# Kernel tuning notes

Hardware: AMD Instinct MI355X
Metric: run time of the kernel (lower is better)

Reference implementation:

```python
import jax, jax.numpy as jnp
import numpy as np

IMG_SIZE = 640
STRIDES = (8, 16, 32)
KA = 3          # anchors per level
C = 80          # num classes
CONF_THRESH = 0.001
NMS_THRESH = 0.6
TOPK = 4096     # fixed candidate cap for jit-compatible NMS


def setup_inputs() -> dict:
    key = jax.random.key(0)
    k1, k2, k3 = jax.random.split(key, 3)
    ch = KA * (1 + C + 4)  # 255
    pred_s = jax.random.normal(k1, (ch, 80, 80), dtype=jnp.float32)
    pred_m = jax.random.normal(k2, (ch, 40, 40), dtype=jnp.float32)
    pred_l = jax.random.normal(k3, (ch, 20, 20), dtype=jnp.float32)
    # classic YOLOv3 anchors, [level, anchor, (w,h)]
    anchor_size = jnp.array(
        [[[10, 13], [16, 30], [33, 23]],
         [[30, 61], [62, 45], [59, 119]],
         [[116, 90], [156, 198], [373, 326]]], dtype=jnp.float32)
    return {"pred_s": pred_s, "pred_m": pred_m, "pred_l": pred_l,
            "anchor_size": anchor_size}


def _decode_level(pred, anchors, stride):
    # pred: [KA*(1+C+4), H, W]; anchors: [KA, 2]
    H, W = pred.shape[1], pred.shape[2]
    p = jnp.transpose(pred, (1, 2, 0))                    # [H, W, ch]
    obj = p[..., :KA].reshape(-1, 1)                      # [H*W*KA, 1]
    cls = p[..., KA:KA * (1 + C)].reshape(-1, C)          # [H*W*KA, C]
    reg = p[..., KA * (1 + C):].reshape(H * W, KA, 4)     # [H*W, KA, 4]
    gy, gx = jnp.meshgrid(jnp.arange(H), jnp.arange(W), indexing="ij")
    grid = jnp.stack([gx, gy], -1).reshape(-1, 1, 2).astype(pred.dtype)  # [H*W,1,2]
    # center_sample = False branch
    xy = (jax.nn.sigmoid(reg[..., :2]) + grid) * stride
    wh = jnp.exp(reg[..., 2:]) * anchors[None, :, :]
    box = jnp.concatenate([xy - 0.5 * wh, xy + 0.5 * wh], -1).reshape(-1, 4)
    return obj, cls, box


def _decode(pred_s, pred_m, pred_l, anchor_size):
    parts = [_decode_level(p, anchor_size[i], STRIDES[i])
             for i, p in enumerate([pred_s, pred_m, pred_l])]
    obj = jnp.concatenate([p[0] for p in parts], 0)       # [N,1]
    cls = jnp.concatenate([p[1] for p in parts], 0)       # [N,C]
    box = jnp.concatenate([p[2] for p in parts], 0)       # [N,4]
    bboxes = jnp.clip(box / IMG_SIZE, 0.0, 1.0)
    scores = jax.nn.sigmoid(obj) * jax.nn.softmax(cls, axis=-1)
    return bboxes, scores


def reference(pred_s, pred_m, pred_l, anchor_size):
    bboxes, scores = _decode(pred_s, pred_m, pred_l, anchor_size)
    cls_inds = jnp.argmax(scores, axis=1)                 # [N]
    sc = jnp.max(scores, axis=1)                          # [N]
    sc_masked = jnp.where(sc >= CONF_THRESH, sc, -1.0)
    top_sc, idx = jax.lax.top_k(sc_masked, TOPK)          # candidates, score-sorted
    b = bboxes[idx]                                       # [K,4]
    c = cls_inds[idx]                                     # [K]
    valid = top_sc >= CONF_THRESH                         # [K]
    # pairwise IoU, exactly as the numpy NMS computes it
    x1, y1, x2, y2 = b[:, 0], b[:, 1], b[:, 2], b[:, 3]
    area = (x2 - x1) * (y2 - y1)
    xx1 = jnp.maximum(x1[:, None], x1[None, :])
    yy1 = jnp.maximum(y1[:, None], y1[None, :])
    xx2 = jnp.minimum(x2[:, None], x2[None, :])
    yy2 = jnp.minimum(y2[:, None], y2[None, :])
    w = jnp.maximum(1e-28, xx2 - xx1)
    h = jnp.maximum(1e-28, yy2 - yy1)
    inter = w * h
    iou = inter / (area[:, None] + area[None, :] - inter + 1e-14)
    # sup[j, i] = kept j (earlier in score order) suppresses i, same class only
    order = jnp.arange(TOPK)
    sup = (c[:, None] == c[None, :]) & (iou > NMS_THRESH) \
          & (order[:, None] < order[None, :])
    def body(i, keep):
        ki = valid[i] & ~jnp.any(keep & sup[:, i])
        return keep.at[i].set(ki)
    keep = jax.lax.fori_loop(0, TOPK, body, jnp.zeros(TOPK, dtype=bool))
    return b, top_sc, c, keep
```

## Files before the change

### kernel.cpp

```cpp
#include <hip/hip_runtime.h>
#include <cstdint>
#include <cstddef>

#define N_ANCH 25200
#define NB0 19200
#define NB1 24000
#define TOPK_N 4096
#define CONF_T 0.001
#define NMS_T 0.6
#define IMGS 640.0
#define NBINS 8192
#define JS 16

typedef unsigned long long u64;

struct WS {
  alignas(64) double sc[N_ANCH];
  alignas(64) double box[N_ANCH][4];
  alignas(64) int    cls[N_ANCH];
  alignas(64) int    binv[N_ANCH];
  alignas(64) int    rank[N_ANCH];
  alignas(64) int    subset[N_ANCH];
  alignas(64) double ssc[N_ANCH];
  int    m_count;
  int    t_bin;
  alignas(64) double tbox[TOPK_N][4];
  alignas(64) double tarea[TOPK_N];
  alignas(64) double tsc[TOPK_N];
  alignas(64) int    tcls[TOPK_N];
  alignas(64) u64    supT[TOPK_N * 64];
  alignas(64) u64    hasSup[64];
};

__device__ __forceinline__ double dsigmoid(double x) { return 1.0 / (1.0 + exp(-x)); }

__device__ __forceinline__ int score_bin(double sc) {
  if (sc < 0.0) return 0;
  return (int)(__float_as_uint((float)sc) >> 17);
}

__global__ void k_decode(const float* __restrict__ ps, const float* __restrict__ pm,
                         const float* __restrict__ pl, const float* __restrict__ anch,
                         WS* __restrict__ ws) {
  int tid = blockIdx.x * 256 + threadIdx.x;
  int a = tid >> 2;
  int r = tid & 3;
  if (a >= N_ANCH) return;
  const float* p; int W, base, lvl; double stride;
  if (a < NB0)      { p = ps; W = 80; base = 0;   lvl = 0; stride = 8.0; }
  else if (a < NB1) { p = pm; W = 40; base = NB0; lvl = 1; stride = 16.0; }
  else              { p = pl; W = 20; base = NB1; lvl = 2; stride = 32.0; }
  int e = a - base;
  int pos = e / 3;
  int k = e - 3 * pos;
  int HW = W * W;

  const float* pc = p + (size_t)(3 + k * 80) * HW + pos;
  double m = -1e300, ssum = 0.0; int am = 0;
  for (int t = 0; t < 20; ++t) {
    int c = r + 4 * t;
    double v = (double)pc[(size_t)c * HW];
    ssum += exp(v);
    if (v > m) { m = v; am = c; }
  }
  for (int off = 1; off <= 2; off <<= 1) {
    double om = __shfl_xor(m, off);
    int oam   = __shfl_xor(am, off);
    double os = __shfl_xor(ssum, off);
    ssum += os;
    if (om > m || (om == m && oam < am)) { m = om; am = oam; }
  }

  if (r == 0) {
    double sobj = dsigmoid((double)p[(size_t)k * HW + pos]);
    double sc = sobj * (exp(m) / ssum);

    int x = pos % W, y = pos / W;
    const float* pr = p + (size_t)(243 + k * 4) * HW + pos;
    double tx = (double)pr[0];
    double ty = (double)pr[(size_t)HW];
    double tw = (double)pr[(size_t)2 * HW];
    double th = (double)pr[(size_t)3 * HW];
    double cx = (dsigmoid(tx) + (double)x) * stride;
    double cy = (dsigmoid(ty) + (double)y) * stride;
    double aw = (double)anch[lvl * 6 + k * 2 + 0];
    double ah = (double)anch[lvl * 6 + k * 2 + 1];
    double bw = exp(tw) * aw;
    double bh = exp(th) * ah;
    double x1 = fmin(fmax((cx - 0.5 * bw) / IMGS, 0.0), 1.0);
    double y1 = fmin(fmax((cy - 0.5 * bh) / IMGS, 0.0), 1.0);
    double x2 = fmin(fmax((cx + 0.5 * bw) / IMGS, 0.0), 1.0);
    double y2 = fmin(fmax((cy + 0.5 * bh) / IMGS, 0.0), 1.0);

    ws->box[a][0] = x1; ws->box[a][1] = y1;
    ws->box[a][2] = x2; ws->box[a][3] = y2;
    ws->cls[a] = am;
    double scm = (sc >= CONF_T) ? sc : -1.0;
    ws->sc[a] = scm;
    ws->binv[a] = score_bin(scm);
  }
}

__global__ void __launch_bounds__(1024) k_select(WS* __restrict__ ws) {
  __shared__ int hist[NBINS];
  __shared__ int part[1024];
  int t = threadIdx.x;
  for (int i = t; i < NBINS; i += 1024) hist[i] = 0;
  __syncthreads();
  for (int i = t; i < N_ANCH; i += 1024) atomicAdd(&hist[ws->binv[i]], 1);
  __syncthreads();
  const int CH = NBINS / 1024;
  int sum = 0;
  for (int rr = 0; rr < CH; ++rr) sum += hist[NBINS - 1 - (t * CH + rr)];
  part[t] = sum;
  __syncthreads();
  for (int off = 1; off < 1024; off <<= 1) {
    int v = (t >= off) ? part[t - off] : 0;
    __syncthreads();
    part[t] += v;
    __syncthreads();
  }
  int cum = part[t] - sum;
  for (int rr = 0; rr < CH; ++rr) {
    int b = NBINS - 1 - (t * CH + rr);
    int h = hist[b];
    int prev = cum;
    cum += h;
    if (prev < TOPK_N && cum >= TOPK_N) ws->t_bin = b;
  }
  if (t == 0) ws->m_count = 0;
}

__global__ void k_compact(WS* __restrict__ ws) {
  int i = blockIdx.x * 256 + threadIdx.x;
  if (i < 64) ws->hasSup[i] = 0ull;
  if (i >= N_ANCH) return;
  int tb = ws->t_bin;
  if (ws->binv[i] >= tb) {
    int idx = atomicAdd(&ws->m_count, 1);
    ws->subset[idx] = i;
    ws->ssc[idx] = ws->sc[i];
    ws->rank[idx] = 0;
  }
}

__global__ void k_rank(WS* __restrict__ ws) {
  const int CHUNK = 1024;
  __shared__ double sj[CHUNK];
  __shared__ int    aj[CHUNK];
  int m = ws->m_count;
  if ((int)blockIdx.x * 256 >= m) return;
  int i = blockIdx.x * 256 + threadIdx.x;
  bool active = (i < m);
  int ai = active ? ws->subset[i] : 0;
  double si = active ? ws->ssc[i] : -2.0;

  int jlen = (m + JS - 1) / JS;
  int j0 = blockIdx.y * jlen;
  int jend = min(j0 + jlen, m);
  int cnt = 0;
  for (int jc = j0; jc < jend; jc += CHUNK) {
    int n = min(CHUNK, jend - jc);
    __syncthreads();
    for (int t = threadIdx.x; t < n; t += 256) {
      aj[t] = ws->subset[jc + t];
      sj[t] = ws->ssc[jc + t];
    }
    __syncthreads();
    if (active) {
      for (int t = 0; t < n; ++t) {
        double s = sj[t];
        cnt += (int)((s > si) | ((s == si) & (aj[t] < ai)));
      }
    }
  }
  if (active && cnt) atomicAdd(&ws->rank[i], cnt);
}

__global__ void k_scatter(WS* __restrict__ ws, float* __restrict__ out) {
  int m = ws->m_count;
  int i = blockIdx.x * 256 + threadIdx.x;
  if (i >= m) return;
  int r = ws->rank[i];
  if (r >= TOPK_N) return;
  int a = ws->subset[i];
  double b0 = ws->box[a][0], b1 = ws->box[a][1];
  double b2 = ws->box[a][2], b3 = ws->box[a][3];
  double s  = ws->ssc[i];
  int    c  = ws->cls[a];
  ws->tbox[r][0] = b0; ws->tbox[r][1] = b1;
  ws->tbox[r][2] = b2; ws->tbox[r][3] = b3;
  ws->tarea[r] = (b2 - b0) * (b3 - b1);
  ws->tsc[r] = s;
  ws->tcls[r] = c;
  out[r * 4 + 0] = (float)b0;
  out[r * 4 + 1] = (float)b1;
  out[r * 4 + 2] = (float)b2;
  out[r * 4 + 3] = (float)b3;
  out[4 * TOPK_N + r] = (float)s;
  out[5 * TOPK_N + r] = (float)c;
}

__global__ void k_iou(WS* __restrict__ ws) {
  int tid = threadIdx.x;
  int w = blockIdx.y;
  int i0 = blockIdx.x * 256;
  int jbase = w * 64;
  if (jbase >= i0 + 256) {
    ws->supT[(size_t)(i0 + tid) * 64 + w] = 0ull;
    return;
  }
  __shared__ double jb[64][5];
  __shared__ int jc[64];
  if (tid < 64) {
    int j = jbase + tid;
    jb[tid][0] = ws->tbox[j][0];
    jb[tid][1] = ws->tbox[j][1];
    jb[tid][2] = ws->tbox[j][2];
    jb[tid][3] = ws->tbox[j][3];
    jb[tid][4] = ws->tarea[j];
    jc[tid] = ws->tcls[j];
  }
  __syncthreads();
  int i = i0 + tid;
  double x1 = ws->tbox[i][0], y1 = ws->tbox[i][1];
  double x2 = ws->tbox[i][2], y2 = ws->tbox[i][3];
  double ai = ws->tarea[i];
  int ci = ws->tcls[i];
  u64 bits = 0;
  for (int t = 0; t < 64; ++t) {
    double xx1 = fmax(x1, jb[t][0]);
    double yy1 = fmax(y1, jb[t][1]);
    double xx2 = fmin(x2, jb[t][2]);
    double yy2 = fmin(y2, jb[t][3]);
    double iw = fmax(1e-28, xx2 - xx1);
    double ih = fmax(1e-28, yy2 - yy1);
    double inter = iw * ih;
    double denom = ai + jb[t][4] - inter + 1e-14;
    bool sup = (jc[t] == ci) && (inter > NMS_T * denom) && ((jbase + t) < i);
    bits |= ((u64)sup) << t;
  }
  ws->supT[(size_t)i * 64 + w] = bits;
  if (bits) atomicOr(&ws->hasSup[i >> 6], 1ull << (i & 63));
}

__global__ void __launch_bounds__(64) k_nms(const WS* __restrict__ ws, float* __restrict__ out) {
  __shared__ u64 hsArr[64];
  __shared__ int lst[TOPK_N];
  int lane = threadIdx.x;

  u64 validw = 0;
  const double4* tp = (const double4*)(ws->tsc + lane * 64);
  for (int q = 0; q < 16; ++q) {
    double4 v = tp[q];
    validw |= ((u64)(v.x >= CONF_T)) << (q * 4 + 0);
    validw |= ((u64)(v.y >= CONF_T)) << (q * 4 + 1);
    validw |= ((u64)(v.z >= CONF_T)) << (q * 4 + 2);
    validw |= ((u64)(v.w >= CONF_T)) << (q * 4 + 3);
  }

  u64 hasw = ws->hasSup[lane];
  u64 keepw = validw & ~hasw;
  hsArr[lane] = hasw;
  __syncthreads();

  int K = 0;
  for (int l = 0; l < 64; ++l) {
    u64 w = hsArr[l];
    while (w) {
      int b = __builtin_ctzll(w);
      w &= w - 1;
      if (lane == 0) lst[K] = l * 64 + b;
      ++K;
    }
  }
  __syncthreads();

  const u64* ST = ws->supT;
  int IA[16], IB[16];
  u64 A[16], B[16];

#pragma unroll
  for (int r = 0; r < 16; ++r) IA[r] = (r < K) ? lst[r] : 0;
#pragma unroll
  for (int r = 0; r < 16; ++r) A[r] = (r < K) ? ST[(size_t)IA[r] * 64 + lane] : 0ull;

  for (int base = 0; base < K; base += 32) {
#pragma unroll
    for (int r = 0; r < 16; ++r) IB[r] = (base + 16 + r < K) ? lst[base + 16 + r] : 0;
#pragma unroll
    for (int r = 0; r < 16; ++r) B[r] = (base + 16 + r < K) ? ST[(size_t)IB[r] * 64 + lane] : 0ull;
#pragma unroll
    for (int r = 0; r < 16; ++r) {
      if (base + r < K) {
        int i = IA[r];
        u64 bal = __ballot((keepw & A[r]) != 0ull);
        if (lane == (i >> 6) && bal == 0ull && ((validw >> (i & 63)) & 1ull))
          keepw |= 1ull << (i & 63);
      }
    }
#pragma unroll
    for (int r = 0; r < 16; ++r) IA[r] = (base + 32 + r < K) ? lst[base + 32 + r] : 0;
#pragma unroll
    for (int r = 0; r < 16; ++r) A[r] = (base + 32 + r < K) ? ST[(size_t)IA[r] * 64 + lane] : 0ull;
#pragma unroll
    for (int r = 0; r < 16; ++r) {
      if (base + 16 + r < K) {
        int i = IB[r];
        u64 bal = __ballot((keepw & B[r]) != 0ull);
        if (lane == (i >> 6) && bal == 0ull && ((validw >> (i & 63)) & 1ull))
          keepw |= 1ull << (i & 63);
      }
    }
  }

  for (int b = 0; b < 64; ++b)
    out[6 * TOPK_N + lane * 64 + b] = (float)((keepw >> b) & 1ull);
}

extern "C" void kernel_launch(void* const* d_in, const int* in_sizes, int n_in,
                              void* d_out, int out_size, void* d_ws, size_t ws_size,
                              hipStream_t stream) {
  const float* ps   = (const float*)d_in[0];
  const float* pm   = (const float*)d_in[1];
  const float* pl   = (const float*)d_in[2];
  const float* anch = (const float*)d_in[3];
  float* out = (float*)d_out;
  WS* ws = (WS*)d_ws;

  dim3 blk(256);
  k_decode <<<dim3((N_ANCH * 4 + 255) / 256), blk, 0, stream>>>(ps, pm, pl, anch, ws);
  k_select <<<dim3(1), dim3(1024), 0, stream>>>(ws);
  k_compact<<<dim3((N_ANCH + 255) / 256), blk, 0, stream>>>(ws);
  k_rank   <<<dim3((N_ANCH + 255) / 256, JS), blk, 0, stream>>>(ws);
  k_scatter<<<dim3((N_ANCH + 255) / 256), blk, 0, stream>>>(ws, out);
  k_iou    <<<dim3(TOPK_N / 256, 64), blk, 0, stream>>>(ws);
  k_nms    <<<dim3(1), dim3(64), 0, stream>>>(ws, out);
}
```

Before: 123.6 us.

## Fuse all seven stages into one cooperative persistent kernel with grid syncs

Replaces the seven separate launches (decode, select, compact, rank, scatter, iou, nms) with a single cooperative kernel of 256 blocks that separates phases with grid.sync(). The histogram becomes a two-level one, with per-block shared histograms merged into a global one, and every block redoes the prefix scan to find the threshold bin locally. The rank stage is remapped so each thread handles up to three candidates. This targets the launch overhead and the gaps between the many small dependent kernels, at the cost of grid-wide barriers and lower parallelism in the decode and rank phases.

```diff
diff --git a/kernel.cpp b/kernel.cpp
--- a/kernel.cpp
+++ b/kernel.cpp
@@ -1,6 +1,9 @@
 #include <hip/hip_runtime.h>
+#include <hip/hip_cooperative_groups.h>
 #include <cstdint>
 #include <cstddef>
+
+namespace cg = cooperative_groups;
 
 #define N_ANCH 25200
 #define NB0 19200
@@ -10,7 +13,8 @@
 #define NMS_T 0.6
 #define IMGS 640.0
 #define NBINS 8192
-#define JS 16
+#define GRID_B 256
+#define NTHR (GRID_B * 256)
 
 typedef unsigned long long u64;
 
@@ -22,8 +26,8 @@
   alignas(64) int    rank[N_ANCH];
   alignas(64) int    subset[N_ANCH];
   alignas(64) double ssc[N_ANCH];
+  alignas(64) int    hist[NBINS];
   int    m_count;
-  int    t_bin;
   alignas(64) double tbox[TOPK_N][4];
   alignas(64) double tarea[TOPK_N];
   alignas(64) double tsc[TOPK_N];
@@ -39,283 +43,307 @@
   return (int)(__float_as_uint((float)sc) >> 17);
 }
 
-__global__ void k_decode(const float* __restrict__ ps, const float* __restrict__ pm,
-                         const float* __restrict__ pl, const float* __restrict__ anch,
-                         WS* __restrict__ ws) {
-  int tid = blockIdx.x * 256 + threadIdx.x;
-  int a = tid >> 2;
-  int r = tid & 3;
-  if (a >= N_ANCH) return;
-  const float* p; int W, base, lvl; double stride;
-  if (a < NB0)      { p = ps; W = 80; base = 0;   lvl = 0; stride = 8.0; }
-  else if (a < NB1) { p = pm; W = 40; base = NB0; lvl = 1; stride = 16.0; }
-  else              { p = pl; W = 20; base = NB1; lvl = 2; stride = 32.0; }
-  int e = a - base;
-  int pos = e / 3;
-  int k = e - 3 * pos;
-  int HW = W * W;
-
-  const float* pc = p + (size_t)(3 + k * 80) * HW + pos;
-  double m = -1e300, ssum = 0.0; int am = 0;
-  for (int t = 0; t < 20; ++t) {
-    int c = r + 4 * t;
-    double v = (double)pc[(size_t)c * HW];
-    ssum += exp(v);
-    if (v > m) { m = v; am = c; }
-  }
-  for (int off = 1; off <= 2; off <<= 1) {
-    double om = __shfl_xor(m, off);
-    int oam   = __shfl_xor(am, off);
-    double os = __shfl_xor(ssum, off);
-    ssum += os;
-    if (om > m || (om == m && oam < am)) { m = om; am = oam; }
-  }
-
-  if (r == 0) {
-    double sobj = dsigmoid((double)p[(size_t)k * HW + pos]);
-    double sc = sobj * (exp(m) / ssum);
-
-    int x = pos % W, y = pos / W;
-    const float* pr = p + (size_t)(243 + k * 4) * HW + pos;
-    double tx = (double)pr[0];
-    double ty = (double)pr[(size_t)HW];
-    double tw = (double)pr[(size_t)2 * HW];
-    double th = (double)pr[(size_t)3 * HW];
-    double cx = (dsigmoid(tx) + (double)x) * stride;
-    double cy = (dsigmoid(ty) + (double)y) * stride;
-    double aw = (double)anch[lvl * 6 + k * 2 + 0];
-    double ah = (double)anch[lvl * 6 + k * 2 + 1];
-    double bw = exp(tw) * aw;
-    double bh = exp(th) * ah;
-    double x1 = fmin(fmax((cx - 0.5 * bw) / IMGS, 0.0), 1.0);
-    double y1 = fmin(fmax((cy - 0.5 * bh) / IMGS, 0.0), 1.0);
-    double x2 = fmin(fmax((cx + 0.5 * bw) / IMGS, 0.0), 1.0);
-    double y2 = fmin(fmax((cy + 0.5 * bh) / IMGS, 0.0), 1.0);
-
-    ws->box[a][0] = x1; ws->box[a][1] = y1;
-    ws->box[a][2] = x2; ws->box[a][3] = y2;
-    ws->cls[a] = am;
-    double scm = (sc >= CONF_T) ? sc : -1.0;
-    ws->sc[a] = scm;
-    ws->binv[a] = score_bin(scm);
-  }
-}
-
-__global__ void __launch_bounds__(1024) k_select(WS* __restrict__ ws) {
-  __shared__ int hist[NBINS];
-  __shared__ int part[1024];
-  int t = threadIdx.x;
-  for (int i = t; i < NBINS; i += 1024) hist[i] = 0;
+struct SelSmem { int hist[NBINS]; int part[256]; };
+struct RankSmem { double sj[2048]; int aj[2048]; };
+struct IouSmem { double jb[64][5]; int jc[64]; };
+struct NmsSmem { u64 hs[64]; int lst[TOPK_N]; };
+
+__global__ void __launch_bounds__(256)
+k_fused(const float* __restrict__ ps, const float* __restrict__ pm,
+        const float* __restrict__ pl, const float* __restrict__ anch,
+        WS* __restrict__ ws, float* __restrict__ out) {
+  cg::grid_group grid = cg::this_grid();
+  __shared__ union { SelSmem sel; RankSmem rk; IouSmem iou; NmsSmem nms; } sm;
+  __shared__ int s_tbin;
+
+  const int t = threadIdx.x;
+  const int gtid = blockIdx.x * 256 + t;
+
+  for (int b = gtid; b < NBINS; b += NTHR) ws->hist[b] = 0;
+  if (gtid < 64) ws->hasSup[gtid] = 0ull;
+  if (gtid == 64) ws->m_count = 0;
+
+  for (int task = gtid; task < N_ANCH * 4; task += NTHR) {
+    int a = task >> 2;
+    int r = task & 3;
+    const float* p; int W, base, lvl; double stride;
+    if (a < NB0)      { p = ps; W = 80; base = 0;   lvl = 0; stride = 8.0; }
+    else if (a < NB1) { p = pm; W = 40; base = NB0; lvl = 1; stride = 16.0; }
+    else              { p = pl; W = 20; base = NB1; lvl = 2; stride = 32.0; }
+    int e = a - base;
+    int pos = e / 3;
+    int k = e - 3 * pos;
+    int HW = W * W;
+
+    const float* pc = p + (size_t)(3 + k * 80) * HW + pos;
+    double m = -1e300, ssum = 0.0; int am = 0;
+    for (int u = 0; u < 20; ++u) {
+      int c = r + 4 * u;
+      double v = (double)pc[(size_t)c * HW];
+      ssum += exp(v);
+      if (v > m) { m = v; am = c; }
+    }
+    for (int off = 1; off <= 2; off <<= 1) {
+      double om = __shfl_xor(m, off);
+      int oam   = __shfl_xor(am, off);
+      double os = __shfl_xor(ssum, off);
+      ssum += os;
+      if (om > m || (om == m && oam < am)) { m = om; am = oam; }
+    }
+
+    if (r == 0) {
+      double sobj = dsigmoid((double)p[(size_t)k * HW + pos]);
+      double sc = sobj * (exp(m) / ssum);
+
+      int x = pos % W, y = pos / W;
+      const float* pr = p + (size_t)(243 + k * 4) * HW + pos;
+      double tx = (double)pr[0];
+      double ty = (double)pr[(size_t)HW];
+      double tw = (double)pr[(size_t)2 * HW];
+      double th = (double)pr[(size_t)3 * HW];
+      double cx = (dsigmoid(tx) + (double)x) * stride;
+      double cy = (dsigmoid(ty) + (double)y) * stride;
+      double aw = (double)anch[lvl * 6 + k * 2 + 0];
+      double ah = (double)anch[lvl * 6 + k * 2 + 1];
+      double bw = exp(tw) * aw;
+      double bh = exp(th) * ah;
+      double x1 = fmin(fmax((cx - 0.5 * bw) / IMGS, 0.0), 1.0);
+      double y1 = fmin(fmax((cy - 0.5 * bh) / IMGS, 0.0), 1.0);
+      double x2 = fmin(fmax((cx + 0.5 * bw) / IMGS, 0.0), 1.0);
+      double y2 = fmin(fmax((cy + 0.5 * bh) / IMGS, 0.0), 1.0);
+
+      ws->box[a][0] = x1; ws->box[a][1] = y1;
+      ws->box[a][2] = x2; ws->box[a][3] = y2;
+      ws->cls[a] = am;
+      double scm = (sc >= CONF_T) ? sc : -1.0;
+      ws->sc[a] = scm;
+      ws->binv[a] = score_bin(scm);
+    }
+  }
+  grid.sync();
+
+  for (int b = t; b < NBINS; b += 256) sm.sel.hist[b] = 0;
   __syncthreads();
-  for (int i = t; i < N_ANCH; i += 1024) atomicAdd(&hist[ws->binv[i]], 1);
+  if (gtid < N_ANCH) atomicAdd(&sm.sel.hist[ws->binv[gtid]], 1);
   __syncthreads();
-  const int CH = NBINS / 1024;
-  int sum = 0;
-  for (int rr = 0; rr < CH; ++rr) sum += hist[NBINS - 1 - (t * CH + rr)];
-  part[t] = sum;
-  __syncthreads();
-  for (int off = 1; off < 1024; off <<= 1) {
-    int v = (t >= off) ? part[t - off] : 0;
-    __syncthreads();
-    part[t] += v;
-    __syncthreads();
-  }
-  int cum = part[t] - sum;
-  for (int rr = 0; rr < CH; ++rr) {
-    int b = NBINS - 1 - (t * CH + rr);
-    int h = hist[b];
-    int prev = cum;
-    cum += h;
-    if (prev < TOPK_N && cum >= TOPK_N) ws->t_bin = b;
-  }
-  if (t == 0) ws->m_count = 0;
-}
-
-__global__ void k_compact(WS* __restrict__ ws) {
-  int i = blockIdx.x * 256 + threadIdx.x;
-  if (i < 64) ws->hasSup[i] = 0ull;
-  if (i >= N_ANCH) return;
-  int tb = ws->t_bin;
-  if (ws->binv[i] >= tb) {
-    int idx = atomicAdd(&ws->m_count, 1);
-    ws->subset[idx] = i;
-    ws->ssc[idx] = ws->sc[i];
-    ws->rank[idx] = 0;
-  }
-}
-
-__global__ void k_rank(WS* __restrict__ ws) {
-  const int CHUNK = 1024;
-  __shared__ double sj[CHUNK];
-  __shared__ int    aj[CHUNK];
-  int m = ws->m_count;
-  if ((int)blockIdx.x * 256 >= m) return;
-  int i = blockIdx.x * 256 + threadIdx.x;
-  bool active = (i < m);
-  int ai = active ? ws->subset[i] : 0;
-  double si = active ? ws->ssc[i] : -2.0;
-
-  int jlen = (m + JS - 1) / JS;
-  int j0 = blockIdx.y * jlen;
-  int jend = min(j0 + jlen, m);
-  int cnt = 0;
-  for (int jc = j0; jc < jend; jc += CHUNK) {
-    int n = min(CHUNK, jend - jc);
-    __syncthreads();
-    for (int t = threadIdx.x; t < n; t += 256) {
-      aj[t] = ws->subset[jc + t];
-      sj[t] = ws->ssc[jc + t];
-    }
-    __syncthreads();
-    if (active) {
-      for (int t = 0; t < n; ++t) {
-        double s = sj[t];
-        cnt += (int)((s > si) | ((s == si) & (aj[t] < ai)));
-      }
-    }
-  }
-  if (active && cnt) atomicAdd(&ws->rank[i], cnt);
-}
-
-__global__ void k_scatter(WS* __restrict__ ws, float* __restrict__ out) {
-  int m = ws->m_count;
-  int i = blockIdx.x * 256 + threadIdx.x;
-  if (i >= m) return;
-  int r = ws->rank[i];
-  if (r >= TOPK_N) return;
-  int a = ws->subset[i];
-  double b0 = ws->box[a][0], b1 = ws->box[a][1];
-  double b2 = ws->box[a][2], b3 = ws->box[a][3];
-  double s  = ws->ssc[i];
-  int    c  = ws->cls[a];
-  ws->tbox[r][0] = b0; ws->tbox[r][1] = b1;
-  ws->tbox[r][2] = b2; ws->tbox[r][3] = b3;
-  ws->tarea[r] = (b2 - b0) * (b3 - b1);
-  ws->tsc[r] = s;
-  ws->tcls[r] = c;
-  out[r * 4 + 0] = (float)b0;
-  out[r * 4 + 1] = (float)b1;
-  out[r * 4 + 2] = (float)b2;
-  out[r * 4 + 3] = (float)b3;
-  out[4 * TOPK_N + r] = (float)s;
-  out[5 * TOPK_N + r] = (float)c;
-}
-
-__global__ void k_iou(WS* __restrict__ ws) {
-  int tid = threadIdx.x;
-  int w = blockIdx.y;
-  int i0 = blockIdx.x * 256;
-  int jbase = w * 64;
-  if (jbase >= i0 + 256) {
-    ws->supT[(size_t)(i0 + tid) * 64 + w] = 0ull;
-    return;
-  }
-  __shared__ double jb[64][5];
-  __shared__ int jc[64];
-  if (tid < 64) {
-    int j = jbase + tid;
-    jb[tid][0] = ws->tbox[j][0];
-    jb[tid][1] = ws->tbox[j][1];
-    jb[tid][2] = ws->tbox[j][2];
-    jb[tid][3] = ws->tbox[j][3];
-    jb[tid][4] = ws->tarea[j];
-    jc[tid] = ws->tcls[j];
-  }
-  __syncthreads();
-  int i = i0 + tid;
-  double x1 = ws->tbox[i][0], y1 = ws->tbox[i][1];
-  double x2 = ws->tbox[i][2], y2 = ws->tbox[i][3];
-  double ai = ws->tarea[i];
-  int ci = ws->tcls[i];
-  u64 bits = 0;
-  for (int t = 0; t < 64; ++t) {
-    double xx1 = fmax(x1, jb[t][0]);
-    double yy1 = fmax(y1, jb[t][1]);
-    double xx2 = fmin(x2, jb[t][2]);
-    double yy2 = fmin(y2, jb[t][3]);
-    double iw = fmax(1e-28, xx2 - xx1);
-    double ih = fmax(1e-28, yy2 - yy1);
-    double inter = iw * ih;
-    double denom = ai + jb[t][4] - inter + 1e-14;
-    bool sup = (jc[t] == ci) && (inter > NMS_T * denom) && ((jbase + t) < i);
-    bits |= ((u64)sup) << t;
-  }
-  ws->supT[(size_t)i * 64 + w] = bits;
-  if (bits) atomicOr(&ws->hasSup[i >> 6], 1ull << (i & 63));
-}
-
-__global__ void __launch_bounds__(64) k_nms(const WS* __restrict__ ws, float* __restrict__ out) {
-  __shared__ u64 hsArr[64];
-  __shared__ int lst[TOPK_N];
-  int lane = threadIdx.x;
-
-  u64 validw = 0;
-  const double4* tp = (const double4*)(ws->tsc + lane * 64);
-  for (int q = 0; q < 16; ++q) {
-    double4 v = tp[q];
-    validw |= ((u64)(v.x >= CONF_T)) << (q * 4 + 0);
-    validw |= ((u64)(v.y >= CONF_T)) << (q * 4 + 1);
-    validw |= ((u64)(v.z >= CONF_T)) << (q * 4 + 2);
-    validw |= ((u64)(v.w >= CONF_T)) << (q * 4 + 3);
-  }
-
-  u64 hasw = ws->hasSup[lane];
-  u64 keepw = validw & ~hasw;
-  hsArr[lane] = hasw;
-  __syncthreads();
-
-  int K = 0;
-  for (int l = 0; l < 64; ++l) {
-    u64 w = hsArr[l];
-    while (w) {
-      int b = __builtin_ctzll(w);
-      w &= w - 1;
-      if (lane == 0) lst[K] = l * 64 + b;
-      ++K;
-    }
-  }
-  __syncthreads();
-
-  const u64* ST = ws->supT;
-  int IA[16], IB[16];
-  u64 A[16], B[16];
-
-#pragma unroll
-  for (int r = 0; r < 16; ++r) IA[r] = (r < K) ? lst[r] : 0;
-#pragma unroll
-  for (int r = 0; r < 16; ++r) A[r] = (r < K) ? ST[(size_t)IA[r] * 64 + lane] : 0ull;
-
-  for (int base = 0; base < K; base += 32) {
-#pragma unroll
-    for (int r = 0; r < 16; ++r) IB[r] = (base + 16 + r < K) ? lst[base + 16 + r] : 0;
-#pragma unroll
-    for (int r = 0; r < 16; ++r) B[r] = (base + 16 + r < K) ? ST[(size_t)IB[r] * 64 + lane] : 0ull;
-#pragma unroll
-    for (int r = 0; r < 16; ++r) {
-      if (base + r < K) {
-        int i = IA[r];
-        u64 bal = __ballot((keepw & A[r]) != 0ull);
-        if (lane == (i >> 6) && bal == 0ull && ((validw >> (i & 63)) & 1ull))
-          keepw |= 1ull << (i & 63);
-      }
-    }
-#pragma unroll
-    for (int r = 0; r < 16; ++r) IA[r] = (base + 32 + r < K) ? lst[base + 32 + r] : 0;
-#pragma unroll
-    for (int r = 0; r < 16; ++r) A[r] = (base + 32 + r < K) ? ST[(size_t)IA[r] * 64 + lane] : 0ull;
-#pragma unroll
-    for (int r = 0; r < 16; ++r) {
-      if (base + 16 + r < K) {
-        int i = IB[r];
-        u64 bal = __ballot((keepw & B[r]) != 0ull);
-        if (lane == (i >> 6) && bal == 0ull && ((validw >> (i & 63)) & 1ull))
-          keepw |= 1ull << (i & 63);
-      }
-    }
-  }
-
-  for (int b = 0; b < 64; ++b)
-    out[6 * TOPK_N + lane * 64 + b] = (float)((keepw >> b) & 1ull);
+  for (int b = t; b < NBINS; b += 256) {
+    int h = sm.sel.hist[b];
+    if (h) atomicAdd(&ws->hist[b], h);
+  }
+  grid.sync();
+
+  {
+    const int CH = NBINS / 256;
+    int sum = 0;
+    for (int rr = 0; rr < CH; ++rr) sum += ws->hist[NBINS - 1 - (t * CH + rr)];
+    sm.sel.part[t] = sum;
+    __syncthreads();
+    for (int off = 1; off < 256; off <<= 1) {
+      int v = (t >= off) ? sm.sel.part[t - off] : 0;
+      __syncthreads();
+      sm.sel.part[t] += v;
+      __syncthreads();
+    }
+    int cum = sm.sel.part[t] - sum;
+    for (int rr = 0; rr < CH; ++rr) {
+      int b = NBINS - 1 - (t * CH + rr);
+      int h = ws->hist[b];
+      int prev = cum;
+      cum += h;
+      if (prev < TOPK_N && cum >= TOPK_N) s_tbin = b;
+    }
+    __syncthreads();
+    int tbin = s_tbin;
+    if (gtid < N_ANCH) {
+      if (ws->binv[gtid] >= tbin) {
+        int idx = atomicAdd(&ws->m_count, 1);
+        ws->subset[idx] = gtid;
+        ws->ssc[idx] = ws->sc[gtid];
+        ws->rank[idx] = 0;
+      }
+    }
+  }
+  grid.sync();
+
+  {
+    int m = ws->m_count;
+    int bi = blockIdx.x >> 4;
+    int bj = blockIdx.x & 15;
+    int jlen = (m + 15) >> 4;
+    int j0 = bj * jlen;
+    int jend = min(m, j0 + jlen);
+    int i0 = bi * 256 + t, i1 = i0 + 4096, i2 = i1 + 4096;
+    bool a0 = i0 < m, a1 = i1 < m, a2 = i2 < m;
+    double s0 = a0 ? ws->ssc[i0] : 0.0;  int x0 = a0 ? ws->subset[i0] : 0;
+    double s1 = a1 ? ws->ssc[i1] : 0.0;  int x1 = a1 ? ws->subset[i1] : 0;
+    double s2 = a2 ? ws->ssc[i2] : 0.0;  int x2 = a2 ? ws->subset[i2] : 0;
+    bool p1 = (m > 4096), p2 = (m > 8192);
+    int c0 = 0, c1 = 0, c2 = 0;
+    for (int jc = j0; jc < jend; jc += 2048) {
+      int n = min(2048, jend - jc);
+      __syncthreads();
+      for (int u = t; u < n; u += 256) {
+        sm.rk.sj[u] = ws->ssc[jc + u];
+        sm.rk.aj[u] = ws->subset[jc + u];
+      }
+      __syncthreads();
+      for (int u = 0; u < n; ++u) {
+        double s = sm.rk.sj[u]; int aa = sm.rk.aj[u];
+        c0 += (int)((s > s0) | ((s == s0) & (aa < x0)));
+      }
+      if (p1) for (int u = 0; u < n; ++u) {
+        double s = sm.rk.sj[u]; int aa = sm.rk.aj[u];
+        c1 += (int)((s > s1) | ((s == s1) & (aa < x1)));
+      }
+      if (p2) for (int u = 0; u < n; ++u) {
+        double s = sm.rk.sj[u]; int aa = sm.rk.aj[u];
+        c2 += (int)((s > s2) | ((s == s2) & (aa < x2)));
+      }
+    }
+    if (a0 && c0) atomicAdd(&ws->rank[i0], c0);
+    if (a1 && c1) atomicAdd(&ws->rank[i1], c1);
+    if (a2 && c2) atomicAdd(&ws->rank[i2], c2);
+  }
+  grid.sync();
+
+  {
+    int m = ws->m_count;
+    for (int i = gtid; i < m; i += NTHR) {
+      int r = ws->rank[i];
+      if (r < TOPK_N) {
+        int a = ws->subset[i];
+        double b0 = ws->box[a][0], b1 = ws->box[a][1];
+        double b2 = ws->box[a][2], b3 = ws->box[a][3];
+        double s  = ws->ssc[i];
+        int    c  = ws->cls[a];
+        ws->tbox[r][0] = b0; ws->tbox[r][1] = b1;
+        ws->tbox[r][2] = b2; ws->tbox[r][3] = b3;
+        ws->tarea[r] = (b2 - b0) * (b3 - b1);
+        ws->tsc[r] = s;
+        ws->tcls[r] = c;
+        out[r * 4 + 0] = (float)b0;
+        out[r * 4 + 1] = (float)b1;
+        out[r * 4 + 2] = (float)b2;
+        out[r * 4 + 3] = (float)b3;
+        out[4 * TOPK_N + r] = (float)s;
+        out[5 * TOPK_N + r] = (float)c;
+      }
+    }
+  }
+  grid.sync();
+
+  for (int tile = blockIdx.x; tile < 16 * 64; tile += GRID_B) {
+    int ti = tile >> 6, w = tile & 63;
+    int i0b = ti * 256, jbase = w * 64;
+    int i = i0b + t;
+    if (jbase >= i0b + 256) {
+      ws->supT[(size_t)i * 64 + w] = 0ull;
+      continue;
+    }
+    __syncthreads();
+    if (t < 64) {
+      int j = jbase + t;
+      sm.iou.jb[t][0] = ws->tbox[j][0];
+      sm.iou.jb[t][1] = ws->tbox[j][1];
+      sm.iou.jb[t][2] = ws->tbox[j][2];
+      sm.iou.jb[t][3] = ws->tbox[j][3];
+      sm.iou.jb[t][4] = ws->tarea[j];
+      sm.iou.jc[t] = ws->tcls[j];
+    }
+    __syncthreads();
+    double x1 = ws->tbox[i][0], y1 = ws->tbox[i][1];
+    double x2 = ws->tbox[i][2], y2 = ws->tbox[i][3];
+    double ai = ws->tarea[i];
+    int ci = ws->tcls[i];
+    u64 bits = 0;
+    for (int u = 0; u < 64; ++u) {
+      double xx1 = fmax(x1, sm.iou.jb[u][0]);
+      double yy1 = fmax(y1, sm.iou.jb[u][1]);
+      double xx2 = fmin(x2, sm.iou.jb[u][2]);
+      double yy2 = fmin(y2, sm.iou.jb[u][3]);
+      double iw = fmax(1e-28, xx2 - xx1);
+      double ih = fmax(1e-28, yy2 - yy1);
+      double inter = iw * ih;
+      double denom = ai + sm.iou.jb[u][4] - inter + 1e-14;
+      bool sup = (sm.iou.jc[u] == ci) && (inter > NMS_T * denom) && ((jbase + u) < i);
+      bits |= ((u64)sup) << u;
+    }
+    ws->supT[(size_t)i * 64 + w] = bits;
+    if (bits) atomicOr(&ws->hasSup[i >> 6], 1ull << (i & 63));
+  }
+  grid.sync();
+
+  if (blockIdx.x == 0) {
+    u64 validw = 0, keepw = 0, hasw = 0;
+    if (t < 64) {
+      const double4* tp = (const double4*)(ws->tsc + t * 64);
+      for (int q = 0; q < 16; ++q) {
+        double4 v = tp[q];
+        validw |= ((u64)(v.x >= CONF_T)) << (q * 4 + 0);
+        validw |= ((u64)(v.y >= CONF_T)) << (q * 4 + 1);
+        validw |= ((u64)(v.z >= CONF_T)) << (q * 4 + 2);
+        validw |= ((u64)(v.w >= CONF_T)) << (q * 4 + 3);
+      }
+      hasw = ws->hasSup[t];
+      keepw = validw & ~hasw;
+      sm.nms.hs[t] = hasw;
+    }
+    __syncthreads();
+    int K = 0;
+    if (t < 64) {
+      for (int l = 0; l < 64; ++l) {
+        u64 w = sm.nms.hs[l];
+        while (w) {
+          int b = __builtin_ctzll(w);
+          w &= w - 1;
+          if (t == 0) sm.nms.lst[K] = l * 64 + b;
+          ++K;
+        }
+      }
+    }
+    __syncthreads();
+    if (t < 64) {
+      const u64* ST = ws->supT;
+      const int* lst = sm.nms.lst;
+      int IA[16], IB[16];
+      u64 A[16], B[16];
+#pragma unroll
+      for (int r = 0; r < 16; ++r) IA[r] = (r < K) ? lst[r] : 0;
+#pragma unroll
+      for (int r = 0; r < 16; ++r) A[r] = (r < K) ? ST[(size_t)IA[r] * 64 + t] : 0ull;
+
+      for (int base = 0; base < K; base += 32) {
+#pragma unroll
+        for (int r = 0; r < 16; ++r) IB[r] = (base + 16 + r < K) ? lst[base + 16 + r] : 0;
+#pragma unroll
+        for (int r = 0; r < 16; ++r) B[r] = (base + 16 + r < K) ? ST[(size_t)IB[r] * 64 + t] : 0ull;
+#pragma unroll
+        for (int r = 0; r < 16; ++r) {
+          if (base + r < K) {
+            int i = IA[r];
+            u64 bal = __ballot((keepw & A[r]) != 0ull);
+            if (t == (i >> 6) && bal == 0ull && ((validw >> (i & 63)) & 1ull))
+              keepw |= 1ull << (i & 63);
+          }
+        }
+#pragma unroll
+        for (int r = 0; r < 16; ++r) IA[r] = (base + 32 + r < K) ? lst[base + 32 + r] : 0;
+#pragma unroll
+        for (int r = 0; r < 16; ++r) A[r] = (base + 32 + r < K) ? ST[(size_t)IA[r] * 64 + t] : 0ull;
+#pragma unroll
+        for (int r = 0; r < 16; ++r) {
+          if (base + 16 + r < K) {
+            int i = IB[r];
+            u64 bal = __ballot((keepw & B[r]) != 0ull);
+            if (t == (i >> 6) && bal == 0ull && ((validw >> (i & 63)) & 1ull))
+              keepw |= 1ull << (i & 63);
+          }
+        }
+      }
+      for (int b = 0; b < 64; ++b)
+        out[6 * TOPK_N + t * 64 + b] = (float)((keepw >> b) & 1ull);
+    }
+  }
 }
 
 extern "C" void kernel_launch(void* const* d_in, const int* in_sizes, int n_in,
@@ -328,12 +356,6 @@
   float* out = (float*)d_out;
   WS* ws = (WS*)d_ws;
 
-  dim3 blk(256);
-  k_decode <<<dim3((N_ANCH * 4 + 255) / 256), blk, 0, stream>>>(ps, pm, pl, anch, ws);
-  k_select <<<dim3(1), dim3(1024), 0, stream>>>(ws);
-  k_compact<<<dim3((N_ANCH + 255) / 256), blk, 0, stream>>>(ws);
-  k_rank   <<<dim3((N_ANCH + 255) / 256, JS), blk, 0, stream>>>(ws);
-  k_scatter<<<dim3((N_ANCH + 255) / 256), blk, 0, stream>>>(ws, out);
-  k_iou    <<<dim3(TOPK_N / 256, 64), blk, 0, stream>>>(ws);
-  k_nms    <<<dim3(1), dim3(64), 0, stream>>>(ws, out);
+  void* args[] = { (void*)&ps, (void*)&pm, (void*)&pl, (void*)&anch, (void*)&ws, (void*)&out };
+  hipLaunchCooperativeKernel((void*)k_fused, dim3(GRID_B), dim3(256), args, 0, stream);
 }
```

Result: slower. 315.9 us (+155.7%).

## Fuse select with compact and rank with scatter to cut kernel launches

Applied to the files above, without the earlier changes.

Merges the histogram threshold selection and the compaction into one single-block kernel, and merges the rank counting and scatter into one kernel that holds each candidate's full rank in a register. Two launches and the rank array plus its atomics go away. In exchange, compaction now runs on a single 1024-thread block, and ranking drops the 16-way j-split, so each block scans all m candidates serially with fewer blocks overall.

```diff
diff --git a/kernel.cpp b/kernel.cpp
--- a/kernel.cpp
+++ b/kernel.cpp
@@ -10,7 +10,6 @@
 #define NMS_T 0.6
 #define IMGS 640.0
 #define NBINS 8192
-#define JS 16
 
 typedef unsigned long long u64;
 
@@ -19,11 +18,9 @@
   alignas(64) double box[N_ANCH][4];
   alignas(64) int    cls[N_ANCH];
   alignas(64) int    binv[N_ANCH];
-  alignas(64) int    rank[N_ANCH];
   alignas(64) int    subset[N_ANCH];
   alignas(64) double ssc[N_ANCH];
   int    m_count;
-  int    t_bin;
   alignas(64) double tbox[TOPK_N][4];
   alignas(64) double tarea[TOPK_N];
   alignas(64) double tsc[TOPK_N];
@@ -101,10 +98,13 @@
   }
 }
 
-__global__ void __launch_bounds__(1024) k_select(WS* __restrict__ ws) {
+__global__ void __launch_bounds__(1024) k_selcomp(WS* __restrict__ ws) {
   __shared__ int hist[NBINS];
   __shared__ int part[1024];
+  __shared__ int s_tbin;
   int t = threadIdx.x;
+  if (t == 0) ws->m_count = 0;
+  if (t < 64) ws->hasSup[t] = 0ull;
   for (int i = t; i < NBINS; i += 1024) hist[i] = 0;
   __syncthreads();
   for (int i = t; i < N_ANCH; i += 1024) atomicAdd(&hist[ws->binv[i]], 1);
@@ -126,79 +126,64 @@
     int h = hist[b];
     int prev = cum;
     cum += h;
-    if (prev < TOPK_N && cum >= TOPK_N) ws->t_bin = b;
-  }
-  if (t == 0) ws->m_count = 0;
-}
-
-__global__ void k_compact(WS* __restrict__ ws) {
-  int i = blockIdx.x * 256 + threadIdx.x;
-  if (i < 64) ws->hasSup[i] = 0ull;
-  if (i >= N_ANCH) return;
-  int tb = ws->t_bin;
-  if (ws->binv[i] >= tb) {
-    int idx = atomicAdd(&ws->m_count, 1);
-    ws->subset[idx] = i;
-    ws->ssc[idx] = ws->sc[i];
-    ws->rank[idx] = 0;
-  }
-}
-
-__global__ void k_rank(WS* __restrict__ ws) {
-  const int CHUNK = 1024;
+    if (prev < TOPK_N && cum >= TOPK_N) s_tbin = b;
+  }
+  __syncthreads();
+  int tbin = s_tbin;
+  for (int i = t; i < N_ANCH; i += 1024) {
+    if (ws->binv[i] >= tbin) {
+      int idx = atomicAdd(&ws->m_count, 1);
+      ws->subset[idx] = i;
+      ws->ssc[idx] = ws->sc[i];
+    }
+  }
+}
+
+__global__ void k_rankscatter(WS* __restrict__ ws, float* __restrict__ out) {
+  const int CHUNK = 2048;
   __shared__ double sj[CHUNK];
   __shared__ int    aj[CHUNK];
   int m = ws->m_count;
   if ((int)blockIdx.x * 256 >= m) return;
-  int i = blockIdx.x * 256 + threadIdx.x;
+  int t = threadIdx.x;
+  int i = blockIdx.x * 256 + t;
   bool active = (i < m);
   int ai = active ? ws->subset[i] : 0;
   double si = active ? ws->ssc[i] : -2.0;
 
-  int jlen = (m + JS - 1) / JS;
-  int j0 = blockIdx.y * jlen;
-  int jend = min(j0 + jlen, m);
   int cnt = 0;
-  for (int jc = j0; jc < jend; jc += CHUNK) {
-    int n = min(CHUNK, jend - jc);
+  for (int jc = 0; jc < m; jc += CHUNK) {
+    int n = min(CHUNK, m - jc);
     __syncthreads();
-    for (int t = threadIdx.x; t < n; t += 256) {
-      aj[t] = ws->subset[jc + t];
-      sj[t] = ws->ssc[jc + t];
+    for (int u = t; u < n; u += 256) {
+      aj[u] = ws->subset[jc + u];
+      sj[u] = ws->ssc[jc + u];
     }
     __syncthreads();
     if (active) {
-      for (int t = 0; t < n; ++t) {
-        double s = sj[t];
-        cnt += (int)((s > si) | ((s == si) & (aj[t] < ai)));
+      for (int u = 0; u < n; ++u) {
+        double s = sj[u];
+        cnt += (int)((s > si) | ((s == si) & (aj[u] < ai)));
       }
     }
   }
-  if (active && cnt) atomicAdd(&ws->rank[i], cnt);
-}
-
-__global__ void k_scatter(WS* __restrict__ ws, float* __restrict__ out) {
-  int m = ws->m_count;
-  int i = blockIdx.x * 256 + threadIdx.x;
-  if (i >= m) return;
-  int r = ws->rank[i];
-  if (r >= TOPK_N) return;
-  int a = ws->subset[i];
-  double b0 = ws->box[a][0], b1 = ws->box[a][1];
-  double b2 = ws->box[a][2], b3 = ws->box[a][3];
-  double s  = ws->ssc[i];
-  int    c  = ws->cls[a];
-  ws->tbox[r][0] = b0; ws->tbox[r][1] = b1;
-  ws->tbox[r][2] = b2; ws->tbox[r][3] = b3;
-  ws->tarea[r] = (b2 - b0) * (b3 - b1);
-  ws->tsc[r] = s;
-  ws->tcls[r] = c;
-  out[r * 4 + 0] = (float)b0;
-  out[r * 4 + 1] = (float)b1;
-  out[r * 4 + 2] = (float)b2;
-  out[r * 4 + 3] = (float)b3;
-  out[4 * TOPK_N + r] = (float)s;
-  out[5 * TOPK_N + r] = (float)c;
+  if (active && cnt < TOPK_N) {
+    int r = cnt;
+    double b0 = ws->box[ai][0], b1 = ws->box[ai][1];
+    double b2 = ws->box[ai][2], b3 = ws->box[ai][3];
+    int    c  = ws->cls[ai];
+    ws->tbox[r][0] = b0; ws->tbox[r][1] = b1;
+    ws->tbox[r][2] = b2; ws->tbox[r][3] = b3;
+    ws->tarea[r] = (b2 - b0) * (b3 - b1);
+    ws->tsc[r] = si;
+    ws->tcls[r] = c;
+    out[r * 4 + 0] = (float)b0;
+    out[r * 4 + 1] = (float)b1;
+    out[r * 4 + 2] = (float)b2;
+    out[r * 4 + 3] = (float)b3;
+    out[4 * TOPK_N + r] = (float)si;
+    out[5 * TOPK_N + r] = (float)c;
+  }
 }
 
 __global__ void k_iou(WS* __restrict__ ws) {
@@ -329,11 +314,9 @@
   WS* ws = (WS*)d_ws;
 
   dim3 blk(256);
-  k_decode <<<dim3((N_ANCH * 4 + 255) / 256), blk, 0, stream>>>(ps, pm, pl, anch, ws);
-  k_select <<<dim3(1), dim3(1024), 0, stream>>>(ws);
-  k_compact<<<dim3((N_ANCH + 255) / 256), blk, 0, stream>>>(ws);
-  k_rank   <<<dim3((N_ANCH + 255) / 256, JS), blk, 0, stream>>>(ws);
-  k_scatter<<<dim3((N_ANCH + 255) / 256), blk, 0, stream>>>(ws, out);
-  k_iou    <<<dim3(TOPK_N / 256, 64), blk, 0, stream>>>(ws);
-  k_nms    <<<dim3(1), dim3(64), 0, stream>>>(ws, out);
-}
+  k_decode     <<<dim3((N_ANCH * 4 + 255) / 256), blk, 0, stream>>>(ps, pm, pl, anch, ws);
+  k_selcomp    <<<dim3(1), dim3(1024), 0, stream>>>(ws);
+  k_rankscatter<<<dim3((N_ANCH + 255) / 256), blk, 0, stream>>>(ws, out);
+  k_iou        <<<dim3(TOPK_N / 256, 64), blk, 0, stream>>>(ws);
+  k_nms        <<<dim3(1), dim3(64), 0, stream>>>(ws, out);
+}
```

Result: slower. 232.8 us (+88.4%).
